# Optimization experiments

Measured on AMD Instinct MI355X. Metric: run time of the kernel, lower is better.

The kernel has to match this reference:

```python
import jax, jax.numpy as jnp
import numpy as np

N = 20000   # nodes
E = 400000  # edges per hop
IN_C = 256
HID = 128
HEADS = 2
OUT_C = 256
RELU_SLOPE = 0.2  # GATConv LeakyReLU negative slope
EPS = 1e-16


def _segment_mean(vals, idx, num_segments):
    s = jax.ops.segment_sum(vals, idx, num_segments=num_segments)
    cnt = jax.ops.segment_sum(jnp.ones((vals.shape[0], 1), vals.dtype), idx,
                              num_segments=num_segments)
    return s / (cnt + EPS)


def _gat(x, src, dst, Wg, a_src, a_dst, bg):
    # x: [N, IN_C] -> h: [N, HEADS, HID]
    h = (x @ Wg).reshape(N, HEADS, HID)
    alpha_s = jnp.sum(h * a_src, axis=-1)  # [N, HEADS]
    alpha_d = jnp.sum(h * a_dst, axis=-1)  # [N, HEADS]
    logits = jax.nn.leaky_relu(alpha_s[src] + alpha_d[dst], RELU_SLOPE)  # [E, HEADS]
    # softmax over incoming edges per destination node
    m = jax.ops.segment_max(logits, dst, num_segments=N)  # [N, HEADS]
    m = jnp.where(jnp.isfinite(m), m, 0.0)
    ex = jnp.exp(logits - m[dst])
    denom = jax.ops.segment_sum(ex, dst, num_segments=N)  # [N, HEADS]
    alpha = ex / (denom[dst] + EPS)  # [E, HEADS]
    msg = h[src] * alpha[..., None]  # [E, HEADS, HID]
    out = jax.ops.segment_sum(msg, dst, num_segments=N)  # [N, HEADS, HID]
    return out.reshape(N, HEADS * HID) + bg


def setup_inputs() -> dict:
    key = jax.random.key(0)
    ks = jax.random.split(key, 16)

    def xav(k, shape):
        fan_in, fan_out = shape[0], shape[-1]
        lim = np.sqrt(6.0 / (fan_in + fan_out)).astype(np.float32)
        return jax.random.uniform(k, shape, jnp.float32, -lim, lim)

    inp = {
        "x": jax.random.normal(ks[0], (N, IN_C), jnp.float32),
        "edge_index_1hop": jax.random.randint(ks[1], (2, E), 0, N),
        "edge_time_1hop": jax.random.uniform(ks[2], (E,), jnp.float32),
        "edge_index_2hop": jax.random.randint(ks[3], (2, E), 0, N),
        "edge_time_2hop": jax.random.uniform(ks[4], (E,), jnp.float32),
        "rel_embeddings": jax.random.normal(ks[5], (N, HID), jnp.float32),
        # GATConv params
        "Wg": xav(ks[6], (IN_C, HEADS * HID)),
        "a_src": jax.random.normal(ks[7], (HEADS, HID), jnp.float32) * 0.1,
        "a_dst": jax.random.normal(ks[8], (HEADS, HID), jnp.float32) * 0.1,
        "bg": jnp.zeros((HEADS * HID,), jnp.float32),
        # linear_transform
        "W_lin": xav(ks[9], (HEADS * HID, OUT_C)),
        "b_lin": jnp.zeros((OUT_C,), jnp.float32),
        # time_gate: in = 2*(OUT_C+1)
        "W_tg": xav(ks[10], (2 * (OUT_C + 1), 1)),
        "b_tg": jnp.zeros((1,), jnp.float32),
        # semantic_gate: in = (OUT_C+1) + HID + 1
        "W_sg": xav(ks[11], (OUT_C + 1 + HID + 1, 1)),
        "b_sg": jnp.zeros((1,), jnp.float32),
    }
    return inp


def reference(x, edge_index_1hop, edge_time_1hop, edge_index_2hop,
              edge_time_2hop, rel_embeddings, Wg, a_src, a_dst, bg,
              W_lin, b_lin, W_tg, b_tg, W_sg, b_sg):
    src1, dst1 = edge_index_1hop[0], edge_index_1hop[1]
    src2, dst2 = edge_index_2hop[0], edge_index_2hop[1]

    # ---- 1-hop aggregation ----
    x_1hop = _gat(x, src1, dst1, Wg, a_src, a_dst, bg) @ W_lin + b_lin  # [N, OUT_C]
    time_e1 = edge_time_1hop[:, None]  # [E, 1]
    node_time = _segment_mean(time_e1, dst1, N)  # [N, 1]
    x_1hop_t = jnp.concatenate([x_1hop, node_time], axis=-1)  # [N, OUT_C+1]

    # ---- semantic gate (per 1-hop edge -> per node) ----
    combined = jnp.concatenate(
        [x_1hop_t[src1], rel_embeddings[dst1], time_e1], axis=-1)  # [E, OUT_C+1+HID+1]
    sem_w_edge = jax.nn.sigmoid(combined @ W_sg + b_sg)  # [E, 1]
    sem_w_node = _segment_mean(sem_w_edge, dst1, N)  # [N, 1]

    # ---- 2-hop aggregation, semantically weighted ----
    x_2hop = _gat(x, src2, dst2, Wg, a_src, a_dst, bg) @ W_lin + b_lin  # [N, OUT_C]
    x_2hop = x_2hop * sem_w_node
    x_2hop_t = jnp.concatenate([x_2hop, node_time], axis=-1)  # [N, OUT_C+1]

    # ---- time-gated fusion ----
    gate_in = jnp.concatenate([x_1hop_t, x_2hop_t], axis=-1)  # [N, 2*(OUT_C+1)]
    g = jax.nn.sigmoid(gate_in @ W_tg + b_tg)  # [N, 1]
    return g * x_2hop_t + (1.0 - g) * x_1hop_t
```

## Files before the change

kernel.cpp:

```cpp
#include <hip/hip_runtime.h>
#include <math.h>

constexpr float EPSF = 1e-16f;
#define MAXDEG 64
#define BINCH 4096
#define NBUCK 64

typedef __attribute__((ext_vector_type(8))) short bfrag;
typedef __attribute__((ext_vector_type(4))) float ffrag;
typedef __attribute__((ext_vector_type(8))) unsigned short ushortv8;

__device__ __forceinline__ float leaky(float v){ return v >= 0.f ? v : 0.2f*v; }

__device__ __forceinline__ ushort f2bf(float f){
  union { float f; unsigned u; } v; v.f = f;
  unsigned r = (v.u + 0x7FFFu + ((v.u >> 16) & 1u)) >> 16;
  return (ushort)r;
}
__device__ __forceinline__ float bf2f(ushort u){
  union { unsigned u; float f; } v; v.u = ((unsigned)u) << 16;
  return v.f;
}

__device__ __forceinline__ float wred_max(float v){
  #pragma unroll
  for (int d = 32; d; d >>= 1) v = fmaxf(v, __shfl_xor(v, d));
  return v;
}
__device__ __forceinline__ float wred_sum(float v){
  #pragma unroll
  for (int d = 32; d; d >>= 1) v += __shfl_xor(v, d);
  return v;
}


__global__ __launch_bounds__(256) void k_prep(const float* __restrict__ Wg, const float* __restrict__ Wlin,
    const float* __restrict__ rel, const float* __restrict__ Wsg, const float* __restrict__ x,
    ushort* __restrict__ Wgt, ushort* __restrict__ Wlt, ushort* __restrict__ xb, float* __restrict__ p2,
    float4* __restrict__ zbase, int znum4, int ZB, int CB, int N){
  __shared__ float tile[32][33];
  int b = blockIdx.x, t = threadIdx.x;
  if (b < ZB){
    int idx = b*256 + t;
    if (idx < znum4) zbase[idx] = make_float4(0.f,0.f,0.f,0.f);
  } else if (b < ZB + 128){
    int bb = b - ZB;
    const float* W = (bb < 64) ? Wg : Wlin;
    ushort* Wt = (bb < 64) ? Wgt : Wlt;
    bb &= 63;
    int bx = (bb & 7)*32, by = (bb >> 3)*32;
    int tx = t & 31, ty = t >> 5;
    for (int r = ty; r < 32; r += 8) tile[r][tx] = W[(size_t)(by+r)*256 + bx+tx];
    __syncthreads();
    for (int r = ty; r < 32; r += 8) Wt[(size_t)(bx+r)*256 + by+tx] = f2bf(tile[tx][r]);
  } else if (b < ZB + 128 + CB){
    size_t base = ((size_t)(b - ZB - 128)*256 + t) * 8;
    if (base < (size_t)N*256){
      float4 u0 = *(const float4*)(x + base);
      float4 u1 = *(const float4*)(x + base + 4);
      ushortv8 o;
      o[0] = f2bf(u0.x); o[1] = f2bf(u0.y); o[2] = f2bf(u0.z); o[3] = f2bf(u0.w);
      o[4] = f2bf(u1.x); o[5] = f2bf(u1.y); o[6] = f2bf(u1.z); o[7] = f2bf(u1.w);
      *(ushortv8*)(xb + base) = o;
    }
  } else {
    int node = (b-ZB-128-CB)*4 + (t>>6);
    if (node >= N) return;
    int lane = t & 63;
    const float* rr = rel + (size_t)node*128;
    float q = rr[lane]*Wsg[257+lane] + rr[64+lane]*Wsg[321+lane];
    q = wred_sum(q);
    if (lane == 0) p2[node] = q;
  }
}


__global__ __launch_bounds__(256) void k_work1(const ushort* __restrict__ xb, const ushort* __restrict__ Wgt,
    const float* __restrict__ a_src, const float* __restrict__ a_dst,
    ushort* __restrict__ hb, float* __restrict__ as_, float* __restrict__ ad_,
    const int* __restrict__ ei1, const float* __restrict__ et1, const int* __restrict__ ei2,
    int* __restrict__ gcur, int2* __restrict__ bkt1, int2* __restrict__ bkt2,
    int cap1, int cap2, int N, int E1, int E2, int GB1, int B1, int NB){
  __shared__ int hist[NBUCK];
  __shared__ int loff[NBUCK+1];
  __shared__ int cur[NBUCK];
  __shared__ int gbase_s[NBUCK];
  __shared__ int2 stage[BINCH];
  int bid = blockIdx.x, t = threadIdx.x;
  if (bid >= GB1){
    int hop = (bid >= GB1 + B1);
    int cb  = hop ? (bid - GB1 - B1) : (bid - GB1);
    const int* src_arr = hop ? ei2 : ei1;
    const int* dst_arr = hop ? (ei2 + E2) : (ei1 + E1);
    int Eh = hop ? E2 : E1;
    int c0 = cb * BINCH;
    int M = Eh - c0; if (M > BINCH) M = BINCH;
    if (t < NBUCK) hist[t] = 0;
    __syncthreads();
    #pragma unroll
    for (int k = 0; k < BINCH/256; k++){
      int i = k*256 + t;
      if (i < M) atomicAdd(&hist[dst_arr[c0 + i] / NB], 1);
    }
    __syncthreads();
    if (t < NBUCK){
      int v = hist[t];
      int xx = v;
      #pragma unroll
      for (int d = 1; d < NBUCK; d <<= 1){
        int y = __shfl_up(xx, d);
        if (t >= d) xx += y;
      }
      loff[t+1] = xx;
      if (t == 0) loff[0] = 0;
      cur[t] = xx - v;
      gbase_s[t] = atomicAdd(&gcur[hop*NBUCK + t], v);
    }
    __syncthreads();
    #pragma unroll
    for (int k = 0; k < BINCH/256; k++){
      int i = k*256 + t;
      if (i < M){
        int s = src_arr[c0 + i];
        int d = dst_arr[c0 + i];
        int bb = d / NB;
        int ld = d - bb*NB;
        int pos = atomicAdd(&cur[bb], 1);
        float tv = hop ? 0.f : et1[c0 + i];
        stage[pos] = make_int2(s | (ld << 15), __float_as_int(tv));
      }
    }
    __syncthreads();
    int2* bkt = hop ? bkt2 : bkt1;
    int cap = hop ? cap2 : cap1;
    for (int s = t; s < M; s += 256){
      int lo = 0, hi = NBUCK;
      while (hi - lo > 1){ int mid = (lo + hi) >> 1; if (loff[mid] <= s) lo = mid; else hi = mid; }
      int gpos = gbase_s[lo] + (s - loff[lo]);
      if (gpos < cap) bkt[(size_t)lo*cap + gpos] = stage[s];
    }
    return;
  }
  int head = bid & 1;
  int bx = bid >> 1;
  int wid = t >> 6, lane = t & 63;
  int wr = wid >> 1, wc = wid & 1;
  int row0 = bx*128 + wr*64;
  int col0 = head*128 + wc*64;
  int l15 = lane & 15, lk = lane >> 4;
  ffrag acc[4][4];
  #pragma unroll
  for (int i = 0; i < 4; i++)
    #pragma unroll
    for (int j = 0; j < 4; j++){ ffrag z; z[0]=0.f; z[1]=0.f; z[2]=0.f; z[3]=0.f; acc[i][j] = z; }
  for (int kk = 0; kk < 256; kk += 32){
    bfrag a[4], b[4];
    #pragma unroll
    for (int i = 0; i < 4; i++){
      int r = row0 + i*16 + l15; if (r > N-1) r = N-1;
      a[i] = *(const bfrag*)(xb + (size_t)r*256 + kk + lk*8);
      int c = col0 + i*16 + l15;
      b[i] = *(const bfrag*)(Wgt + (size_t)c*256 + kk + lk*8);
    }
    #pragma unroll
    for (int i = 0; i < 4; i++)
      #pragma unroll
      for (int j = 0; j < 4; j++)
        acc[i][j] = __builtin_amdgcn_mfma_f32_16x16x32_bf16(a[i], b[j], acc[i][j], 0, 0, 0);
  }
  float asv[4], adv[4];
  #pragma unroll
  for (int j = 0; j < 4; j++){
    int cc = wc*64 + j*16 + l15;
    asv[j] = a_src[head*128 + cc];
    adv[j] = a_dst[head*128 + cc];
  }
  #pragma unroll
  for (int i = 0; i < 4; i++){
    float ps[4] = {0.f,0.f,0.f,0.f}, pd[4] = {0.f,0.f,0.f,0.f};
    #pragma unroll
    for (int j = 0; j < 4; j++){
      int c = col0 + j*16 + l15;
      #pragma unroll
      for (int q = 0; q < 4; q++){
        int r = row0 + i*16 + lk*4 + q;
        float v = acc[i][j][q];
        if (r < N) hb[(size_t)r*256 + c] = f2bf(v);
        ps[q] = fmaf(v, asv[j], ps[q]);
        pd[q] = fmaf(v, adv[j], pd[q]);
      }
    }
    #pragma unroll
    for (int q = 0; q < 4; q++){
      #pragma unroll
      for (int d = 1; d < 16; d <<= 1){
        ps[q] += __shfl_xor(ps[q], d);
        pd[q] += __shfl_xor(pd[q], d);
      }
      int r = row0 + i*16 + lk*4 + q;
      if (l15 == 0 && r < N){
        atomicAdd(&as_[r*2 + head], ps[q]);
        atomicAdd(&ad_[r*2 + head], pd[q]);
      }
    }
  }
}


__global__ __launch_bounds__(256) void k_place(const int* __restrict__ gcur,
    const int2* __restrict__ bkt1, const int2* __restrict__ bkt2, int cap1, int cap2,
    int* __restrict__ ssrc1, int* __restrict__ ssrc2, float* __restrict__ stime1,
    int* __restrict__ cntg, float* __restrict__ ntime, float* __restrict__ p1,
    const float* __restrict__ Wsg, int N, int NB){
  __shared__ int   cnt_l[512];
  __shared__ float ts_l[512];
  int b = blockIdx.x & 63, hop = blockIdx.x >> 6;
  int t = threadIdx.x;
  int nbase = b * NB;
  int ncnt = N - nbase; if (ncnt > NB) ncnt = NB; if (ncnt < 0) ncnt = 0;
  for (int i = t; i < NB; i += 256){ cnt_l[i] = 0; ts_l[i] = 0.f; }
  __syncthreads();
  const int2* bkt = hop ? bkt2 : bkt1;
  int cap = hop ? cap2 : cap1;
  int len = gcur[hop*NBUCK + b]; if (len > cap) len = cap;
  int* ssrc = hop ? ssrc2 : ssrc1;
  for (int i = t; i < len; i += 256){
    int2 en = bkt[(size_t)b*cap + i];
    int src = en.x & 0x7FFF;
    int ld  = en.x >> 15;
    int slot = atomicAdd(&cnt_l[ld], 1);
    if (slot < MAXDEG){
      size_t o = (size_t)(nbase + ld)*MAXDEG + slot;
      ssrc[o] = src;
      if (hop == 0) stime1[o] = __int_as_float(en.y);
    }
    if (hop == 0) atomicAdd(&ts_l[ld], __int_as_float(en.y));
  }
  __syncthreads();
  float w256 = Wsg[256];
  for (int ld = t; ld < ncnt; ld += 256){
    int node = nbase + ld;
    int c = cnt_l[ld];
    cntg[hop*N + node] = c;
    if (hop == 0){
      float nt = ts_l[ld] / ((float)c + EPSF);
      ntime[node] = nt;
      p1[node] = nt * w256;
    }
  }
}


__global__ __launch_bounds__(256) void k_node(const int* __restrict__ cntg,
    const int* __restrict__ ssrc1, const int* __restrict__ ssrc2,
    const float* __restrict__ as_, const float* __restrict__ ad_,
    const ushort* __restrict__ h, const float* __restrict__ bg,
    ushort* __restrict__ gatb, int N, int gN4){
  __shared__ int   s_src[4][MAXDEG];
  __shared__ float2 s_w[4][MAXDEG];
  int wid = threadIdx.x >> 6, lane = threadIdx.x & 63;
  int hop = blockIdx.x >= gN4;
  int node = (blockIdx.x - (hop ? gN4 : 0))*4 + wid;
  bool active = node < N;
  const int* ssrc = hop ? ssrc2 : ssrc1;
  int deg = 0; float ad0 = 0.f, ad1 = 0.f;
  if (active){
    int degt = cntg[hop*N + node];
    deg = degt > MAXDEG ? MAXDEG : degt;
    ad0 = ad_[node*2]; ad1 = ad_[node*2+1];
  }
  size_t o0 = (size_t)node * MAXDEG;
  int msrc = 0;
  float l0 = -INFINITY, l1 = -INFINITY;
  if (lane < deg){
    msrc = ssrc[o0 + lane];
    float2 a = ((const float2*)as_)[msrc];
    l0 = leaky(a.x + ad0); l1 = leaky(a.y + ad1);
  }
  float m0 = wred_max(l0), m1 = wred_max(l1);
  float x0 = 0.f, x1 = 0.f;
  if (lane < deg){ x0 = __expf(l0 - m0); x1 = __expf(l1 - m1); }
  float e0 = wred_sum(x0), e1 = wred_sum(x1);
  float rd0 = 1.f/(e0 + EPSF), rd1 = 1.f/(e1 + EPSF);
  s_src[wid][lane] = msrc;
  s_w[wid][lane] = make_float2(x0*rd0, x1*rd1);
  if (!active) return;
  int eh = lane >> 5, cl = lane & 31, ch0 = cl << 3, head = cl >> 4;
  const int* srow = s_src[wid];
  float acc[8] = {0.f,0.f,0.f,0.f,0.f,0.f,0.f,0.f};
  int i = 0;
  for (; i + 8 <= deg; i += 8){
    int eA = i + eh, eB = i + 2 + eh, eC = i + 4 + eh, eD = i + 6 + eh;
    int sA = srow[eA], sB = srow[eB], sC = srow[eC], sD = srow[eD];
    float2 wA2 = s_w[wid][eA], wB2 = s_w[wid][eB];
    float2 wC2 = s_w[wid][eC], wD2 = s_w[wid][eD];
    float wA = head ? wA2.y : wA2.x;
    float wB = head ? wB2.y : wB2.x;
    float wC = head ? wC2.y : wC2.x;
    float wD = head ? wD2.y : wD2.x;
    ushortv8 uA = *(const ushortv8*)(h + (size_t)sA*256 + ch0);
    ushortv8 uB = *(const ushortv8*)(h + (size_t)sB*256 + ch0);
    ushortv8 uC = *(const ushortv8*)(h + (size_t)sC*256 + ch0);
    ushortv8 uD = *(const ushortv8*)(h + (size_t)sD*256 + ch0);
    #pragma unroll
    for (int k = 0; k < 8; k++) acc[k] = fmaf(wA, bf2f(uA[k]), acc[k]);
    #pragma unroll
    for (int k = 0; k < 8; k++) acc[k] = fmaf(wB, bf2f(uB[k]), acc[k]);
    #pragma unroll
    for (int k = 0; k < 8; k++) acc[k] = fmaf(wC, bf2f(uC[k]), acc[k]);
    #pragma unroll
    for (int k = 0; k < 8; k++) acc[k] = fmaf(wD, bf2f(uD[k]), acc[k]);
  }
  for (; i + 4 <= deg; i += 4){
    int eA = i + eh, eB = i + 2 + eh;
    int sA = srow[eA], sB = srow[eB];
    float2 wA2 = s_w[wid][eA], wB2 = s_w[wid][eB];
    float wA = head ? wA2.y : wA2.x;
    float wB = head ? wB2.y : wB2.x;
    ushortv8 uA = *(const ushortv8*)(h + (size_t)sA*256 + ch0);
    ushortv8 uB = *(const ushortv8*)(h + (size_t)sB*256 + ch0);
    #pragma unroll
    for (int k = 0; k < 8; k++) acc[k] = fmaf(wA, bf2f(uA[k]), acc[k]);
    #pragma unroll
    for (int k = 0; k < 8; k++) acc[k] = fmaf(wB, bf2f(uB[k]), acc[k]);
  }
  for (; i < deg; i += 2){
    int e = i + eh;
    bool v = e < deg;
    int s = v ? srow[e] : 0;
    float w = 0.f;
    if (v){ float2 w2 = s_w[wid][e]; w = head ? w2.y : w2.x; }
    ushortv8 u = *(const ushortv8*)(h + (size_t)s*256 + ch0);
    #pragma unroll
    for (int k = 0; k < 8; k++) acc[k] = fmaf(w, bf2f(u[k]), acc[k]);
  }
  #pragma unroll
  for (int k = 0; k < 8; k++) acc[k] += __shfl_xor(acc[k], 32);
  if (eh == 0){
    float4 b0 = *(const float4*)(bg + ch0);
    float4 b1 = *(const float4*)(bg + ch0 + 4);
    ushortv8 o;
    o[0] = f2bf(acc[0] + b0.x); o[1] = f2bf(acc[1] + b0.y);
    o[2] = f2bf(acc[2] + b0.z); o[3] = f2bf(acc[3] + b0.w);
    o[4] = f2bf(acc[4] + b1.x); o[5] = f2bf(acc[5] + b1.y);
    o[6] = f2bf(acc[6] + b1.z); o[7] = f2bf(acc[7] + b1.w);
    *(ushortv8*)(gatb + (size_t)(hop ? N + node : node)*256 + ch0) = o;
  }
}


__global__ __launch_bounds__(256) void k_gemm2(const ushort* __restrict__ A, const ushort* __restrict__ Bt,
    const float* __restrict__ bias, const float* __restrict__ Wsg,
    ushort* __restrict__ Cb, float* __restrict__ p1, int M, int N){
  int wid = threadIdx.x >> 6, lane = threadIdx.x & 63;
  int wr = wid >> 1, wc = wid & 1;
  int row0 = blockIdx.x*128 + wr*64;
  int col0 = blockIdx.y*128 + wc*64;
  int l15 = lane & 15, lk = lane >> 4;
  ffrag acc[4][4];
  #pragma unroll
  for (int i = 0; i < 4; i++)
    #pragma unroll
    for (int j = 0; j < 4; j++){ ffrag z; z[0]=0.f; z[1]=0.f; z[2]=0.f; z[3]=0.f; acc[i][j] = z; }
  for (int kk = 0; kk < 256; kk += 32){
    bfrag a[4], b[4];
    #pragma unroll
    for (int i = 0; i < 4; i++){
      int r = row0 + i*16 + l15; if (r > M-1) r = M-1;
      a[i] = *(const bfrag*)(A + (size_t)r*256 + kk + lk*8);
      int c = col0 + i*16 + l15;
      b[i] = *(const bfrag*)(Bt + (size_t)c*256 + kk + lk*8);
    }
    #pragma unroll
    for (int i = 0; i < 4; i++)
      #pragma unroll
      for (int j = 0; j < 4; j++)
        acc[i][j] = __builtin_amdgcn_mfma_f32_16x16x32_bf16(a[i], b[j], acc[i][j], 0, 0, 0);
  }
  float wsv[4]; float bv[4];
  #pragma unroll
  for (int j = 0; j < 4; j++){
    int c = col0 + j*16 + l15;
    wsv[j] = Wsg[c];
    bv[j] = bias[c];
  }
  #pragma unroll
  for (int i = 0; i < 4; i++){
    float ps[4] = {0.f,0.f,0.f,0.f};
    #pragma unroll
    for (int j = 0; j < 4; j++){
      int c = col0 + j*16 + l15;
      #pragma unroll
      for (int q = 0; q < 4; q++){
        int r = row0 + i*16 + lk*4 + q;
        float v = acc[i][j][q] + bv[j];
        if (r < M) Cb[(size_t)r*256 + c] = f2bf(v);
        ps[q] = fmaf(v, wsv[j], ps[q]);
      }
    }
    #pragma unroll
    for (int q = 0; q < 4; q++){
      #pragma unroll
      for (int d = 1; d < 16; d <<= 1) ps[q] += __shfl_xor(ps[q], d);
      int r = row0 + i*16 + lk*4 + q;
      if (l15 == 0 && r < N) atomicAdd(&p1[r], ps[q]);
    }
  }
}


__global__ __launch_bounds__(256) void k_final(const ushort* __restrict__ x1, const ushort* __restrict__ x2r,
    const int* __restrict__ cntg, const int* __restrict__ ssrc1, const float* __restrict__ stime1,
    const float* __restrict__ p1, const float* __restrict__ p2,
    const float* __restrict__ Wsg, const float* __restrict__ bsg,
    const float* __restrict__ ntime, const float* __restrict__ Wtg, const float* __restrict__ btg,
    float* __restrict__ out, int N){
  int node = blockIdx.x*4 + (threadIdx.x>>6);
  if (node >= N) return;
  int lane = threadIdx.x & 63;
  int degt = cntg[node];
  int deg = degt > MAXDEG ? MAXDEG : degt;
  float acc = 0.f;
  if (lane < deg){
    size_t o = (size_t)node*MAXDEG + lane;
    float z = p1[ssrc1[o]] + p2[node] + bsg[0] + stime1[o]*Wsg[385];
    acc = 1.f / (1.f + __expf(-z));
  }
  acc = wred_sum(acc);
  float sm = acc / ((float)degt + EPSF);
  float nt = ntime[node];
  int c0 = lane << 2;
  ushort4 au = *(const ushort4*)(x1  + (size_t)node*256 + c0);
  ushort4 ru = *(const ushort4*)(x2r + (size_t)node*256 + c0);
  float4 a4 = make_float4(bf2f(au.x), bf2f(au.y), bf2f(au.z), bf2f(au.w));
  float4 b4; b4.x = bf2f(ru.x)*sm; b4.y = bf2f(ru.y)*sm; b4.z = bf2f(ru.z)*sm; b4.w = bf2f(ru.w)*sm;
  float4 w1 = *(const float4*)(Wtg + c0);
  float4 w2 = *(const float4*)(Wtg + 257 + c0);
  float s = a4.x*w1.x + a4.y*w1.y + a4.z*w1.z + a4.w*w1.w
          + b4.x*w2.x + b4.y*w2.y + b4.z*w2.z + b4.w*w2.w;
  if (lane == 0) s += nt*Wtg[256] + nt*Wtg[513] + btg[0];
  s = wred_sum(s);
  float g = 1.f / (1.f + __expf(-s));
  float* orow = out + (size_t)node*257;
  orow[c0+0] = g*b4.x + (1.f - g)*a4.x;
  orow[c0+1] = g*b4.y + (1.f - g)*a4.y;
  orow[c0+2] = g*b4.z + (1.f - g)*a4.z;
  orow[c0+3] = g*b4.w + (1.f - g)*a4.w;
  if (lane == 0) orow[256] = nt;
}


extern "C" void kernel_launch(void* const* d_in, const int* in_sizes, int n_in,
                              void* d_out, int out_size, void* d_ws, size_t ws_size,
                              hipStream_t stream){
  const float* x    = (const float*)d_in[0];
  const int*   ei1  = (const int*)d_in[1];
  const float* et1  = (const float*)d_in[2];
  const int*   ei2  = (const int*)d_in[3];
  const float* rel  = (const float*)d_in[5];
  const float* Wg   = (const float*)d_in[6];
  const float* asrc = (const float*)d_in[7];
  const float* adst = (const float*)d_in[8];
  const float* bg   = (const float*)d_in[9];
  const float* Wlin = (const float*)d_in[10];
  const float* blin = (const float*)d_in[11];
  const float* Wtg  = (const float*)d_in[12];
  const float* btg  = (const float*)d_in[13];
  const float* Wsg  = (const float*)d_in[14];
  const float* bsg  = (const float*)d_in[15];
  float* out = (float*)d_out;

  const int N  = in_sizes[0] / 256;
  const int E1 = in_sizes[1] / 2;
  const int E2 = in_sizes[3] / 2;
  const int NB = (N + NBUCK - 1) / NBUCK;
  const int cap1 = E1/NBUCK + 2048;
  const int cap2 = E2/NBUCK + 2048;

  char* base = (char*)d_ws;
  size_t off = 0;
  auto alloc = [&](size_t bytes)->char*{
    char* p = base + off;
    off += (bytes + 255) & ~(size_t)255;
    return p;
  };
  int*    gcur  = (int*)alloc((size_t)2*NBUCK*4);
  float*  as_   = (float*)alloc((size_t)2*N*4);
  float*  ad_   = (float*)alloc((size_t)2*N*4);
  size_t zero_bytes = off;
  ushort* Wgt   = (ushort*)alloc((size_t)256*256*2);
  ushort* Wlt   = (ushort*)alloc((size_t)256*256*2);
  ushort* xb    = (ushort*)alloc((size_t)N*256*2);
  ushort* hb    = (ushort*)alloc((size_t)N*256*2);
  ushort* gatb  = (ushort*)alloc((size_t)2*N*256*2);
  ushort* x12   = (ushort*)alloc((size_t)2*N*256*2);
  float*  ntime = (float*)alloc((size_t)N*4);
  float*  p1    = (float*)alloc((size_t)N*4);
  float*  p2    = (float*)alloc((size_t)N*4);
  int*    cntg  = (int*)alloc((size_t)2*N*4);
  int*    ssrc1 = (int*)alloc((size_t)N*MAXDEG*4);
  int*    ssrc2 = (int*)alloc((size_t)N*MAXDEG*4);
  float*  stime1= (float*)alloc((size_t)N*MAXDEG*4);
  int2*   bkt1  = (int2*)alloc((size_t)NBUCK*cap1*8);
  int2*   bkt2  = (int2*)alloc((size_t)NBUCK*cap2*8);

  dim3 blk(256);
  int gN4 = (N + 3) / 4;
  int GB1 = ((N + 127) / 128) * 2;
  int B1  = (E1 + BINCH - 1) / BINCH;
  int B2  = (E2 + BINCH - 1) / BINCH;
  int znum4 = (int)(zero_bytes / 16);
  int ZB = (znum4 + 255) / 256;
  int CB = (N*256/8 + 255) / 256;
  dim3 ggemm2((2*N + 127) / 128, 2);

  k_prep<<<ZB + 128 + CB + gN4, blk, 0, stream>>>(Wg, Wlin, rel, Wsg, x, Wgt, Wlt, xb, p2,
                                                  (float4*)d_ws, znum4, ZB, CB, N);
  k_work1<<<GB1 + B1 + B2, blk, 0, stream>>>(xb, Wgt, asrc, adst, hb, as_, ad_,
                                             ei1, et1, ei2, gcur, bkt1, bkt2,
                                             cap1, cap2, N, E1, E2, GB1, B1, NB);
  k_place<<<128, blk, 0, stream>>>(gcur, bkt1, bkt2, cap1, cap2, ssrc1, ssrc2, stime1,
                                   cntg, ntime, p1, Wsg, N, NB);
  k_node<<<2*gN4, blk, 0, stream>>>(cntg, ssrc1, ssrc2, as_, ad_, hb, bg, gatb, N, gN4);
  k_gemm2<<<ggemm2, blk, 0, stream>>>(gatb, Wlt, blin, Wsg, x12, p1, 2*N, N);
  k_final<<<gN4, blk, 0, stream>>>(x12, x12 + (size_t)N*256, cntg, ssrc1, stime1,
                                   p1, p2, Wsg, bsg, ntime, Wtg, btg, out, N);
}
```

Baseline: 148.0 us.

## Widen GEMM blocks to 512 threads covering full 256 columns; tag bucket in staged entries

The two GEMM kernels now use 512-thread blocks with 8 waves laid out as 2x4, so one block covers all 256 output columns instead of splitting columns across blocks. Each A tile is then loaded by one block rather than two, and there are half as many launched blocks. The binning path stores the bucket id in the high bits of each staged entry, replacing a per-element binary search over bucket offsets, and k_place masks the local-dst field to match. This depends on the local index fitting in 9 bits and the bucket in 6. Larger blocks may reduce occupancy or change how waves are scheduled.

```diff
diff --git a/kernel.cpp b/kernel.cpp
--- a/kernel.cpp
+++ b/kernel.cpp
@@ -75,7 +75,7 @@
 }
 
 
-__global__ __launch_bounds__(256) void k_work1(const ushort* __restrict__ xb, const ushort* __restrict__ Wgt,
+__global__ __launch_bounds__(512) void k_work1(const ushort* __restrict__ xb, const ushort* __restrict__ Wgt,
     const float* __restrict__ a_src, const float* __restrict__ a_dst,
     ushort* __restrict__ hb, float* __restrict__ as_, float* __restrict__ ad_,
     const int* __restrict__ ei1, const float* __restrict__ et1, const int* __restrict__ ei2,
@@ -98,8 +98,8 @@
     if (t < NBUCK) hist[t] = 0;
     __syncthreads();
     #pragma unroll
-    for (int k = 0; k < BINCH/256; k++){
-      int i = k*256 + t;
+    for (int k = 0; k < BINCH/512; k++){
+      int i = k*512 + t;
       if (i < M) atomicAdd(&hist[dst_arr[c0 + i] / NB], 1);
     }
     __syncthreads();
@@ -118,8 +118,8 @@
     }
     __syncthreads();
     #pragma unroll
-    for (int k = 0; k < BINCH/256; k++){
-      int i = k*256 + t;
+    for (int k = 0; k < BINCH/512; k++){
+      int i = k*512 + t;
       if (i < M){
         int s = src_arr[c0 + i];
         int d = dst_arr[c0 + i];
@@ -127,26 +127,25 @@
         int ld = d - bb*NB;
         int pos = atomicAdd(&cur[bb], 1);
         float tv = hop ? 0.f : et1[c0 + i];
-        stage[pos] = make_int2(s | (ld << 15), __float_as_int(tv));
+        stage[pos] = make_int2(s | (ld << 15) | (bb << 24), __float_as_int(tv));
       }
     }
     __syncthreads();
     int2* bkt = hop ? bkt2 : bkt1;
     int cap = hop ? cap2 : cap1;
-    for (int s = t; s < M; s += 256){
-      int lo = 0, hi = NBUCK;
-      while (hi - lo > 1){ int mid = (lo + hi) >> 1; if (loff[mid] <= s) lo = mid; else hi = mid; }
-      int gpos = gbase_s[lo] + (s - loff[lo]);
-      if (gpos < cap) bkt[(size_t)lo*cap + gpos] = stage[s];
+    for (int s = t; s < M; s += 512){
+      int2 en = stage[s];
+      int bb = (en.x >> 24) & 63;
+      int gpos = gbase_s[bb] + (s - loff[bb]);
+      if (gpos < cap) bkt[(size_t)bb*cap + gpos] = en;
     }
     return;
   }
-  int head = bid & 1;
-  int bx = bid >> 1;
-  int wid = t >> 6, lane = t & 63;
-  int wr = wid >> 1, wc = wid & 1;
+  int bx = bid;
+  int w = t >> 6, lane = t & 63;
+  int wr = w >> 2, wc = w & 3;
   int row0 = bx*128 + wr*64;
-  int col0 = head*128 + wc*64;
+  int col0 = wc*64;
   int l15 = lane & 15, lk = lane >> 4;
   ffrag acc[4][4];
   #pragma unroll
@@ -169,11 +168,13 @@
         acc[i][j] = __builtin_amdgcn_mfma_f32_16x16x32_bf16(a[i], b[j], acc[i][j], 0, 0, 0);
   }
   float asv[4], adv[4];
+  int hd[4];
   #pragma unroll
   for (int j = 0; j < 4; j++){
-    int cc = wc*64 + j*16 + l15;
-    asv[j] = a_src[head*128 + cc];
-    adv[j] = a_dst[head*128 + cc];
+    int c = col0 + j*16 + l15;
+    asv[j] = a_src[c];
+    adv[j] = a_dst[c];
+    hd[j] = c >> 7;
   }
   #pragma unroll
   for (int i = 0; i < 4; i++){
@@ -190,6 +191,7 @@
         pd[q] = fmaf(v, adv[j], pd[q]);
       }
     }
+    int head = hd[0];
     #pragma unroll
     for (int q = 0; q < 4; q++){
       #pragma unroll
@@ -227,7 +229,7 @@
   for (int i = t; i < len; i += 256){
     int2 en = bkt[(size_t)b*cap + i];
     int src = en.x & 0x7FFF;
-    int ld  = en.x >> 15;
+    int ld  = (en.x >> 15) & 0x1FF;
     int slot = atomicAdd(&cnt_l[ld], 1);
     if (slot < MAXDEG){
       size_t o = (size_t)(nbase + ld)*MAXDEG + slot;
@@ -349,13 +351,14 @@
 }
 
 
-__global__ __launch_bounds__(256) void k_gemm2(const ushort* __restrict__ A, const ushort* __restrict__ Bt,
+__global__ __launch_bounds__(512) void k_gemm2(const ushort* __restrict__ A, const ushort* __restrict__ Bt,
     const float* __restrict__ bias, const float* __restrict__ Wsg,
     ushort* __restrict__ Cb, float* __restrict__ p1, int M, int N){
-  int wid = threadIdx.x >> 6, lane = threadIdx.x & 63;
-  int wr = wid >> 1, wc = wid & 1;
+  int t = threadIdx.x;
+  int w = t >> 6, lane = t & 63;
+  int wr = w >> 2, wc = w & 3;
   int row0 = blockIdx.x*128 + wr*64;
-  int col0 = blockIdx.y*128 + wc*64;
+  int col0 = wc*64;
   int l15 = lane & 15, lk = lane >> 4;
   ffrag acc[4][4];
   #pragma unroll
@@ -506,23 +509,23 @@
 
   dim3 blk(256);
   int gN4 = (N + 3) / 4;
-  int GB1 = ((N + 127) / 128) * 2;
+  int GB1 = (N + 127) / 128;
   int B1  = (E1 + BINCH - 1) / BINCH;
   int B2  = (E2 + BINCH - 1) / BINCH;
   int znum4 = (int)(zero_bytes / 16);
   int ZB = (znum4 + 255) / 256;
   int CB = (N*256/8 + 255) / 256;
-  dim3 ggemm2((2*N + 127) / 128, 2);
+  int gG2 = (2*N + 127) / 128;
 
   k_prep<<<ZB + 128 + CB + gN4, blk, 0, stream>>>(Wg, Wlin, rel, Wsg, x, Wgt, Wlt, xb, p2,
                                                   (float4*)d_ws, znum4, ZB, CB, N);
-  k_work1<<<GB1 + B1 + B2, blk, 0, stream>>>(xb, Wgt, asrc, adst, hb, as_, ad_,
-                                             ei1, et1, ei2, gcur, bkt1, bkt2,
-                                             cap1, cap2, N, E1, E2, GB1, B1, NB);
+  k_work1<<<GB1 + B1 + B2, dim3(512), 0, stream>>>(xb, Wgt, asrc, adst, hb, as_, ad_,
+                                                   ei1, et1, ei2, gcur, bkt1, bkt2,
+                                                   cap1, cap2, N, E1, E2, GB1, B1, NB);
   k_place<<<128, blk, 0, stream>>>(gcur, bkt1, bkt2, cap1, cap2, ssrc1, ssrc2, stime1,
                                    cntg, ntime, p1, Wsg, N, NB);
   k_node<<<2*gN4, blk, 0, stream>>>(cntg, ssrc1, ssrc2, as_, ad_, hb, bg, gatb, N, gN4);
-  k_gemm2<<<ggemm2, blk, 0, stream>>>(gatb, Wlt, blin, Wsg, x12, p1, 2*N, N);
+  k_gemm2<<<gG2, dim3(512), 0, stream>>>(gatb, Wlt, blin, Wsg, x12, p1, 2*N, N);
   k_final<<<gN4, blk, 0, stream>>>(x12, x12 + (size_t)N*256, cntg, ssrc1, stime1,
                                    p1, p2, Wsg, bsg, ntime, Wtg, btg, out, N);
 }
```

After: 149.3 us. About the same (+0.9%).
